# Kernel tuning notes

Hardware: AMD Instinct MI355X
Metric: run time of the kernel (lower is better)

Reference implementation:

```python
import jax, jax.numpy as jnp
import numpy as np

GAP = 7  # average_gap from init
B, T = 4096, 8192


def setup_inputs() -> dict:
    key = jax.random.key(0)
    # prices must be nonzero (Percentage divides by previous price)
    x = jax.random.uniform(key, (B, T), dtype=jnp.float32) + 0.5
    return {"x": x}


def reference(x):
    g = GAP
    prev = x[:, :-1]                               # (B, T-1)
    # Delta then Percentage: (x[t+1]-x[t]) / x[t]
    p = (x[:, 1:] - prev) / prev                   # (B, T-1)
    # Norm: divide by per-sample max(|max|, |min|)
    scale = jnp.maximum(jnp.max(p, axis=1), jnp.abs(jnp.min(p, axis=1)))  # (B,)
    pn = p / scale[:, None]                        # (B, T-1)
    # MovingAverage via cumulative sum (replaces per-step loop)
    c = jnp.cumsum(pn, axis=1)                     # (B, T-1)
    win_sum = c[:, g - 1:] - jnp.pad(c, ((0, 0), (1, 0)))[:, :-g]  # (B, T-g)
    ma = win_sum / g                               # (B, T-g)
    # final concat along feature axis
    return jnp.stack([ma, x[:, :-g]], axis=2)      # (B, T-g, 2)
```

## Files before the change

### kernel.cpp

```cpp
#include <hip/hip_runtime.h>


constexpr int T_LEN = 8192;
constexpr int GAP_  = 7;
constexpr int OUTW  = T_LEN - GAP_;
constexpr int NP    = T_LEN - 1;
constexpr int NTHR  = 512;
constexpr int CH    = 16;
constexpr int ROWF  = OUTW * 2;
constexpr int SEGF  = 8192;

typedef float v2f __attribute__((ext_vector_type(2)));

__global__ __launch_bounds__(NTHR)
void forex_prep_kernel(const float* __restrict__ x, float* __restrict__ out,
                       int n_rows) {
    const int row = blockIdx.x;
    if (row >= n_rows) return;
    const int t = threadIdx.x;

    __shared__ float tile[256 * 33];
    __shared__ float red[NTHR / 64];

    const float* __restrict__ xr = x + (size_t)row * T_LEN;
    const int base = CH * t;

    float xv[CH + GAP_ + 1];
#pragma unroll
    for (int q = 0; q < 6; ++q) {
        const int e = base + 4 * q;
        if (e + 3 < T_LEN) {
            const float4 v = *reinterpret_cast<const float4*>(xr + e);
            xv[4*q+0] = v.x; xv[4*q+1] = v.y; xv[4*q+2] = v.z; xv[4*q+3] = v.w;
        } else {
#pragma unroll
            for (int e2 = 0; e2 < 4; ++e2)
                xv[4*q+e2] = (e + e2 < T_LEN) ? xr[e + e2] : 1.0f;
        }
    }

    float p[CH + GAP_ - 1];
#pragma unroll
    for (int k = 0; k < CH + GAP_ - 1; ++k) {
        const float pk = fmaf(xv[k + 1], __builtin_amdgcn_rcpf(xv[k]), -1.0f);
        p[k] = (base + k < NP) ? pk : 0.0f;
    }

    float m = 0.0f;
#pragma unroll
    for (int k = 0; k < CH; ++k) m = fmaxf(m, fabsf(p[k]));
#pragma unroll
    for (int off = 32; off > 0; off >>= 1)
        m = fmaxf(m, __shfl_xor(m, off, 64));
    if ((t & 63) == 0) red[t >> 6] = m;
    __syncthreads();
    float scale = red[0];
#pragma unroll
    for (int wv = 1; wv < NTHR / 64; ++wv) scale = fmaxf(scale, red[wv]);
    const float inv = __builtin_amdgcn_rcpf(scale * (float)GAP_);

    float ma[CH];
    float w = ((p[0] + p[1]) + (p[2] + p[3])) + ((p[4] + p[5]) + p[6]);
    ma[0] = w * inv;
#pragma unroll
    for (int k = 1; k < CH; ++k) {
        w += p[k + GAP_ - 1] - p[k - 1];
        ma[k] = w * inv;
    }

    const int my_seg = t >> 8;
    const int u = t & 255;
    float* __restrict__ orow = out + (size_t)row * ROWF;

#pragma unroll
    for (int seg = 0; seg < 2; ++seg) {
        if (my_seg == seg) {
            float* tb = tile + 33 * u;
#pragma unroll
            for (int k = 0; k < CH; ++k) {
                tb[2*k]     = ma[k];
                tb[2*k + 1] = xv[k];
            }
        }
        __syncthreads();
        const int nf = (seg == 0) ? SEGF : (ROWF - SEGF);
        float* __restrict__ gb = orow + seg * SEGF;
#pragma unroll
        for (int q = 0; q < 8; ++q) {
            const int L = (q * NTHR + t) * 2;
            if (L < nf) {
                const int Lp = L + (L >> 5);
                const v2f val = {tile[Lp], tile[Lp + 1]};
                __builtin_nontemporal_store(val,
                    reinterpret_cast<v2f*>(gb + L));
            }
        }
        if (seg == 0) __syncthreads();
    }
}

extern "C" void kernel_launch(void* const* d_in, const int* in_sizes, int n_in,
                              void* d_out, int out_size, void* d_ws, size_t ws_size,
                              hipStream_t stream) {
    const float* x = (const float*)d_in[0];
    float* out = (float*)d_out;
    const int n_rows = in_sizes[0] / T_LEN;
    dim3 grid(n_rows), block(NTHR);
    hipLaunchKernelGGL(forex_prep_kernel, grid, block, 0, stream, x, out, n_rows);
}
```

Measured before the change: 73.51 us.

## Use persistent row-strided blocks with register prefetch of the next row

Replaces one-block-per-row with a fixed grid of 512 persistent blocks that loop over rows. Each block prefetches the next row into registers while reducing and storing the current one, so load latency overlaps compute and stores, and per-block launch overhead goes away. The cost is extra register pressure from the doubled input buffer under a 4-blocks-per-CU launch bound, which may cause spills. A fixed grid may also leave CUs imbalanced.

```diff
diff --git a/kernel.cpp b/kernel.cpp
--- a/kernel.cpp
+++ b/kernel.cpp
@@ -9,93 +9,115 @@
 constexpr int CH    = 16;
 constexpr int ROWF  = OUTW * 2;
 constexpr int SEGF  = 8192;
+constexpr int NBLK  = 512;
 
 typedef float v2f __attribute__((ext_vector_type(2)));
 
-__global__ __launch_bounds__(NTHR)
+#define LOAD_ROW(xr, dst)                                                    \
+    {                                                                        \
+        _Pragma("unroll")                                                    \
+        for (int q = 0; q < 6; ++q) {                                        \
+            const int e = base + 4 * q;                                      \
+            if (e + 3 < T_LEN) {                                             \
+                const float4 v = *reinterpret_cast<const float4*>((xr) + e); \
+                dst[4*q+0] = v.x; dst[4*q+1] = v.y;                          \
+                dst[4*q+2] = v.z; dst[4*q+3] = v.w;                          \
+            } else {                                                         \
+                _Pragma("unroll")                                            \
+                for (int e2 = 0; e2 < 4; ++e2)                               \
+                    dst[4*q+e2] = (e + e2 < T_LEN) ? (xr)[e + e2] : 1.0f;    \
+            }                                                                \
+        }                                                                    \
+    }
+
+__global__ __launch_bounds__(NTHR, 4)
 void forex_prep_kernel(const float* __restrict__ x, float* __restrict__ out,
                        int n_rows) {
-    const int row = blockIdx.x;
-    if (row >= n_rows) return;
-    const int t = threadIdx.x;
+    const int t    = threadIdx.x;
+    const int base = CH * t;
 
     __shared__ float tile[256 * 33];
     __shared__ float red[NTHR / 64];
 
-    const float* __restrict__ xr = x + (size_t)row * T_LEN;
-    const int base = CH * t;
+    int row = blockIdx.x;
+    if (row >= n_rows) return;
+    const int stride = gridDim.x;
 
-    float xv[CH + GAP_ + 1];
+    float xv [CH + GAP_ + 1];
+    float nxv[CH + GAP_ + 1];
+    LOAD_ROW(x + (size_t)row * T_LEN, xv);
+
+    for (; row < n_rows; row += stride) {
+        const int nrow = row + stride;
+
+        float p[CH + GAP_ - 1];
 #pragma unroll
-    for (int q = 0; q < 6; ++q) {
-        const int e = base + 4 * q;
-        if (e + 3 < T_LEN) {
-            const float4 v = *reinterpret_cast<const float4*>(xr + e);
-            xv[4*q+0] = v.x; xv[4*q+1] = v.y; xv[4*q+2] = v.z; xv[4*q+3] = v.w;
-        } else {
+        for (int k = 0; k < CH + GAP_ - 1; ++k) {
+            const float pk = fmaf(xv[k + 1], __builtin_amdgcn_rcpf(xv[k]), -1.0f);
+            p[k] = (base + k < NP) ? pk : 0.0f;
+        }
+        float m = 0.0f;
 #pragma unroll
-            for (int e2 = 0; e2 < 4; ++e2)
-                xv[4*q+e2] = (e + e2 < T_LEN) ? xr[e + e2] : 1.0f;
+        for (int k = 0; k < CH; ++k) m = fmaxf(m, fabsf(p[k]));
+
+        if (nrow < n_rows) {
+            const float* xrn = x + (size_t)nrow * T_LEN;
+            LOAD_ROW(xrn, nxv);
         }
-    }
-
-    float p[CH + GAP_ - 1];
-#pragma unroll
-    for (int k = 0; k < CH + GAP_ - 1; ++k) {
-        const float pk = fmaf(xv[k + 1], __builtin_amdgcn_rcpf(xv[k]), -1.0f);
-        p[k] = (base + k < NP) ? pk : 0.0f;
-    }
-
-    float m = 0.0f;
-#pragma unroll
-    for (int k = 0; k < CH; ++k) m = fmaxf(m, fabsf(p[k]));
-#pragma unroll
-    for (int off = 32; off > 0; off >>= 1)
-        m = fmaxf(m, __shfl_xor(m, off, 64));
-    if ((t & 63) == 0) red[t >> 6] = m;
-    __syncthreads();
-    float scale = red[0];
-#pragma unroll
-    for (int wv = 1; wv < NTHR / 64; ++wv) scale = fmaxf(scale, red[wv]);
-    const float inv = __builtin_amdgcn_rcpf(scale * (float)GAP_);
-
-    float ma[CH];
-    float w = ((p[0] + p[1]) + (p[2] + p[3])) + ((p[4] + p[5]) + p[6]);
-    ma[0] = w * inv;
-#pragma unroll
-    for (int k = 1; k < CH; ++k) {
-        w += p[k + GAP_ - 1] - p[k - 1];
-        ma[k] = w * inv;
-    }
-
-    const int my_seg = t >> 8;
-    const int u = t & 255;
-    float* __restrict__ orow = out + (size_t)row * ROWF;
 
 #pragma unroll
-    for (int seg = 0; seg < 2; ++seg) {
-        if (my_seg == seg) {
-            float* tb = tile + 33 * u;
+        for (int off = 32; off > 0; off >>= 1)
+            m = fmaxf(m, __shfl_xor(m, off, 64));
+        if ((t & 63) == 0) red[t >> 6] = m;
+        __syncthreads();
+        float scale = red[0];
 #pragma unroll
-            for (int k = 0; k < CH; ++k) {
-                tb[2*k]     = ma[k];
-                tb[2*k + 1] = xv[k];
+        for (int wv = 1; wv < NTHR / 64; ++wv) scale = fmaxf(scale, red[wv]);
+        const float inv = __builtin_amdgcn_rcpf(scale * (float)GAP_);
+
+        float ma[CH];
+        float w = ((p[0] + p[1]) + (p[2] + p[3])) + ((p[4] + p[5]) + p[6]);
+        ma[0] = w * inv;
+#pragma unroll
+        for (int k = 1; k < CH; ++k) {
+            w += p[k + GAP_ - 1] - p[k - 1];
+            ma[k] = w * inv;
+        }
+
+        const int my_seg = t >> 8;
+        const int u = t & 255;
+        float* __restrict__ orow = out + (size_t)row * ROWF;
+
+#pragma unroll
+        for (int seg = 0; seg < 2; ++seg) {
+            if (my_seg == seg) {
+                float* tb = tile + 33 * u;
+#pragma unroll
+                for (int k = 0; k < CH; ++k) {
+                    tb[2*k]     = ma[k];
+                    tb[2*k + 1] = xv[k];
+                }
             }
+            __syncthreads();
+            const int nf = (seg == 0) ? SEGF : (ROWF - SEGF);
+            float* __restrict__ gb = orow + seg * SEGF;
+#pragma unroll
+            for (int q = 0; q < 8; ++q) {
+                const int L = (q * NTHR + t) * 2;
+                if (L < nf) {
+                    const int Lp = L + (L >> 5);
+                    const v2f val = {tile[Lp], tile[Lp + 1]};
+                    __builtin_nontemporal_store(val,
+                        reinterpret_cast<v2f*>(gb + L));
+                }
+            }
+            __syncthreads();
         }
-        __syncthreads();
-        const int nf = (seg == 0) ? SEGF : (ROWF - SEGF);
-        float* __restrict__ gb = orow + seg * SEGF;
+
+        if (nrow < n_rows) {
 #pragma unroll
-        for (int q = 0; q < 8; ++q) {
-            const int L = (q * NTHR + t) * 2;
-            if (L < nf) {
-                const int Lp = L + (L >> 5);
-                const v2f val = {tile[Lp], tile[Lp + 1]};
-                __builtin_nontemporal_store(val,
-                    reinterpret_cast<v2f*>(gb + L));
-            }
+            for (int e = 0; e < CH + GAP_ + 1; ++e) xv[e] = nxv[e];
         }
-        if (seg == 0) __syncthreads();
     }
 }
 
@@ -105,6 +127,7 @@
     const float* x = (const float*)d_in[0];
     float* out = (float*)d_out;
     const int n_rows = in_sizes[0] / T_LEN;
-    dim3 grid(n_rows), block(NTHR);
-    hipLaunchKernelGGL(forex_prep_kernel, grid, block, 0, stream, x, out, n_rows);
+    const int grid = (n_rows < NBLK) ? n_rows : NBLK;
+    hipLaunchKernelGGL(forex_prep_kernel, dim3(grid), dim3(NTHR), 0, stream,
+                       x, out, n_rows);
 }
```

Measured after the change: 78.04 us. 1.06x slower.
